# Performance work log

Measured on AMD Instinct MI355X. Metric: run time of the kernel, lower is better.

Reference implementation:

```python
import jax, jax.numpy as jnp
import numpy as np

N_NODES = 50000
N_EDGES = 800000
IN_CH = 128
HID = 128   # 2 * out_channels
OUT = 64
LN_EPS = 1e-5
L2_EPS = 1e-12


def setup_inputs() -> dict:
    key = jax.random.key(0)
    ks = jax.random.split(key, 12)
    x = jax.random.normal(ks[0], (N_NODES, IN_CH), dtype=jnp.float32)
    edge_index = jax.random.randint(ks[1], (2, N_EDGES), 0, N_NODES, dtype=jnp.int64)
    # GCNConv weights (glorot-ish scale) + bias; LayerNorm gamma/beta
    W1 = jax.random.normal(ks[2], (IN_CH, HID), dtype=jnp.float32) * (1.0 / np.sqrt(IN_CH))
    b1 = jnp.zeros((HID,), dtype=jnp.float32)
    g1 = jnp.ones((HID,), dtype=jnp.float32)
    beta1 = jnp.zeros((HID,), dtype=jnp.float32)
    W2 = jax.random.normal(ks[3], (HID, OUT), dtype=jnp.float32) * (1.0 / np.sqrt(HID))
    b2 = jnp.zeros((OUT,), dtype=jnp.float32)
    g2 = jnp.ones((OUT,), dtype=jnp.float32)
    beta2 = jnp.zeros((OUT,), dtype=jnp.float32)
    return {"x": x, "edge_index": edge_index, "W1": W1, "b1": b1, "g1": g1,
            "beta1": beta1, "W2": W2, "b2": b2, "g2": g2, "beta2": beta2}


def _layer_norm(h, gamma, beta):
    mu = jnp.mean(h, axis=-1, keepdims=True)
    var = jnp.mean(jnp.square(h - mu), axis=-1, keepdims=True)
    return (h - mu) * jax.lax.rsqrt(var + LN_EPS) * gamma + beta


def reference(x, edge_index, W1, b1, g1, beta1, W2, b2, g2, beta2):
    # Add self-loops once; compute symmetric GCN normalization (shared by both layers).
    loops = jnp.arange(N_NODES, dtype=edge_index.dtype)
    src = jnp.concatenate([edge_index[0], loops])  # [E+N]
    dst = jnp.concatenate([edge_index[1], loops])  # [E+N]
    deg = jax.ops.segment_sum(jnp.ones_like(dst, dtype=x.dtype), dst,
                              num_segments=N_NODES)
    dinv = jnp.where(deg > 0, jax.lax.rsqrt(deg), 0.0)
    norm = dinv[src] * dinv[dst]  # [E+N]

    def gcn_conv(h, W, b):
        h = h @ W                                   # [N, d_out]
        msg = h[src] * norm[:, None]                # gather + scale  [E+N, d_out]
        agg = jax.ops.segment_sum(msg, dst, num_segments=N_NODES)
        return agg + b

    h = jax.nn.relu(_layer_norm(gcn_conv(x, W1, b1), g1, beta1))
    # Dropout(0.4) is identity in eval mode (correctness baseline).
    h = jax.nn.relu(_layer_norm(gcn_conv(h, W2, b2), g2, beta2))
    nrm = jnp.sqrt(jnp.sum(jnp.square(h), axis=1, keepdims=True))
    return h / jnp.maximum(nrm, L2_EPS)
```

## Files before the change

### kernel.cpp

```cpp
#include <hip/hip_runtime.h>
#include <hip/hip_fp16.h>


#define K_DIM 128

__global__ __launch_bounds__(256) void hist_kernel(const int* __restrict__ dst,
                                                   int* counts, int E) {
    int i = blockIdx.x * 256 + threadIdx.x;
    if (i < E) atomicAdd(&counts[dst[i]], 1);
}

__global__ __launch_bounds__(256) void dinv_kernel(const int* __restrict__ counts,
                                                   float* dinv, int n) {
    int i = blockIdx.x * 256 + threadIdx.x;
    if (i < n) dinv[i] = rsqrtf((float)(counts[i] + 1));
}

__global__ __launch_bounds__(256) void scan_block_kernel(const int* __restrict__ counts,
                                                         int* row_ptr, int* partials, int N) {
    __shared__ int sm[256];
    int t = threadIdx.x;
    int i = blockIdx.x * 256 + t;
    int v = (i < N) ? counts[i] : 0;
    sm[t] = v;
    __syncthreads();
    for (int off = 1; off < 256; off <<= 1) {
        int add = (t >= off) ? sm[t - off] : 0;
        __syncthreads();
        sm[t] += add;
        __syncthreads();
    }
    if (i < N) row_ptr[i] = sm[t] - v;
    if (t == 255) partials[blockIdx.x] = sm[255];
}

__global__ __launch_bounds__(256) void scan_partials_kernel(int* partials, int NB) {
    __shared__ int sm[256];
    int t = threadIdx.x;
    int v = (t < NB) ? partials[t] : 0;
    sm[t] = v;
    __syncthreads();
    for (int off = 1; off < 256; off <<= 1) {
        int add = (t >= off) ? sm[t - off] : 0;
        __syncthreads();
        sm[t] += add;
        __syncthreads();
    }
    if (t < NB) partials[t] = sm[t] - v;
}

__global__ __launch_bounds__(256) void scan_add_kernel(int* row_ptr, const int* __restrict__ partials,
                                                       int N) {
    int i = blockIdx.x * 256 + threadIdx.x;
    if (i < N) row_ptr[i] += partials[blockIdx.x];
}

__global__ __launch_bounds__(256) void fill_kernel(const int* __restrict__ src,
                                                   const int* __restrict__ dst,
                                                   const float* __restrict__ dinv,
                                                   int* row_ptr, int* sorted_src,
                                                   float* edge_w, int E) {
    int i = blockIdx.x * 256 + threadIdx.x;
    if (i < E) {
        int d = dst[i];
        int s = src[i];
        int pos = atomicAdd(&row_ptr[d], 1);
        sorted_src[pos] = s;
        edge_w[pos] = dinv[s] * dinv[d];
    }
}

__global__ __launch_bounds__(256) void gemm1_kernel(const float* __restrict__ X,
                                                    const float* __restrict__ W,
                                                    __half* __restrict__ H, int N) {
    constexpr int COLS = 128;
    constexpr int CG = COLS / 4;
    constexpr int RG = 256 / CG;
    constexpr int RT = RG * 4;
    __shared__ float xs[RT][K_DIM + 4];

    int row0 = blockIdx.x * RT;
    for (int idx = threadIdx.x; idx < RT * K_DIM; idx += 256) {
        int r = idx >> 7;
        int c = idx & (K_DIM - 1);
        int row = row0 + r;
        xs[r][c] = (row < N) ? X[(size_t)row * K_DIM + c] : 0.0f;
    }
    __syncthreads();

    int cg = threadIdx.x % CG;
    int rg = threadIdx.x / CG;
    int col = cg * 4;

    float acc[4][4] = {};
    for (int k = 0; k < K_DIM; k += 4) {
        float4 xv0 = *(const float4*)&xs[rg * 4 + 0][k];
        float4 xv1 = *(const float4*)&xs[rg * 4 + 1][k];
        float4 xv2 = *(const float4*)&xs[rg * 4 + 2][k];
        float4 xv3 = *(const float4*)&xs[rg * 4 + 3][k];
#pragma unroll
        for (int kk = 0; kk < 4; ++kk) {
            float4 w = *(const float4*)(W + (size_t)(k + kk) * COLS + col);
            float x0 = (kk == 0) ? xv0.x : (kk == 1) ? xv0.y : (kk == 2) ? xv0.z : xv0.w;
            float x1 = (kk == 0) ? xv1.x : (kk == 1) ? xv1.y : (kk == 2) ? xv1.z : xv1.w;
            float x2 = (kk == 0) ? xv2.x : (kk == 1) ? xv2.y : (kk == 2) ? xv2.z : xv2.w;
            float x3 = (kk == 0) ? xv3.x : (kk == 1) ? xv3.y : (kk == 2) ? xv3.z : xv3.w;
            acc[0][0] = fmaf(x0, w.x, acc[0][0]); acc[0][1] = fmaf(x0, w.y, acc[0][1]);
            acc[0][2] = fmaf(x0, w.z, acc[0][2]); acc[0][3] = fmaf(x0, w.w, acc[0][3]);
            acc[1][0] = fmaf(x1, w.x, acc[1][0]); acc[1][1] = fmaf(x1, w.y, acc[1][1]);
            acc[1][2] = fmaf(x1, w.z, acc[1][2]); acc[1][3] = fmaf(x1, w.w, acc[1][3]);
            acc[2][0] = fmaf(x2, w.x, acc[2][0]); acc[2][1] = fmaf(x2, w.y, acc[2][1]);
            acc[2][2] = fmaf(x2, w.z, acc[2][2]); acc[2][3] = fmaf(x2, w.w, acc[2][3]);
            acc[3][0] = fmaf(x3, w.x, acc[3][0]); acc[3][1] = fmaf(x3, w.y, acc[3][1]);
            acc[3][2] = fmaf(x3, w.z, acc[3][2]); acc[3][3] = fmaf(x3, w.w, acc[3][3]);
        }
    }

#pragma unroll
    for (int r = 0; r < 4; ++r) {
        int row = row0 + rg * 4 + r;
        if (row < N) {
            __half2* o2 = (__half2*)(H + (size_t)row * COLS + col);
            o2[0] = __float22half2_rn(make_float2(acc[r][0], acc[r][1]));
            o2[1] = __float22half2_rn(make_float2(acc[r][2], acc[r][3]));
        }
    }
}

__global__ __launch_bounds__(256) void gather1_fused_kernel(
    const __half* __restrict__ h1, const float* __restrict__ dinv,
    const int* __restrict__ row_ptr, const int* __restrict__ counts,
    const int* __restrict__ sorted_src, const float* __restrict__ edge_w,
    const float* __restrict__ b1, const float* __restrict__ g1,
    const float* __restrict__ beta1, const float* __restrict__ W2,
    __half* __restrict__ h3, int N) {
    __shared__ float lds[4][K_DIM];
    int wave = threadIdx.x >> 6;
    int lane = threadIdx.x & 63;
    int node = blockIdx.x * 4 + wave;
    if (node >= N) return;

    float dd = dinv[node];
    float2 acc = __half22float2(((const __half2*)(h1 + (size_t)node * 128))[lane]);
    acc.x *= dd * dd; acc.y *= dd * dd;

    int end = row_ptr[node];
    int beg = end - counts[node];
    int e = beg;
    for (; e + 4 <= end; e += 4) {
        int s0 = sorted_src[e],     s1 = sorted_src[e + 1];
        int s2 = sorted_src[e + 2], s3 = sorted_src[e + 3];
        float w0 = edge_w[e],     w1 = edge_w[e + 1];
        float w2 = edge_w[e + 2], w3 = edge_w[e + 3];
        __half2 v0 = ((const __half2*)(h1 + (size_t)s0 * 128))[lane];
        __half2 v1 = ((const __half2*)(h1 + (size_t)s1 * 128))[lane];
        __half2 v2 = ((const __half2*)(h1 + (size_t)s2 * 128))[lane];
        __half2 v3 = ((const __half2*)(h1 + (size_t)s3 * 128))[lane];
        float2 f0 = __half22float2(v0), f1 = __half22float2(v1);
        float2 f2 = __half22float2(v2), f3 = __half22float2(v3);
        acc.x = fmaf(f0.x, w0, acc.x); acc.y = fmaf(f0.y, w0, acc.y);
        acc.x = fmaf(f1.x, w1, acc.x); acc.y = fmaf(f1.y, w1, acc.y);
        acc.x = fmaf(f2.x, w2, acc.x); acc.y = fmaf(f2.y, w2, acc.y);
        acc.x = fmaf(f3.x, w3, acc.x); acc.y = fmaf(f3.y, w3, acc.y);
    }
    for (; e < end; ++e) {
        int s = sorted_src[e];
        float w = edge_w[e];
        float2 f = __half22float2(((const __half2*)(h1 + (size_t)s * 128))[lane]);
        acc.x = fmaf(f.x, w, acc.x);
        acc.y = fmaf(f.y, w, acc.y);
    }

    float2 bb = ((const float2*)b1)[lane];
    acc.x += bb.x; acc.y += bb.y;
    float s = acc.x + acc.y;
    for (int off = 32; off; off >>= 1) s += __shfl_xor(s, off);
    float mu = s * (1.0f / 128.0f);
    float dx = acc.x - mu, dy = acc.y - mu;
    float q = dx * dx + dy * dy;
    for (int off = 32; off; off >>= 1) q += __shfl_xor(q, off);
    float rstd = rsqrtf(q * (1.0f / 128.0f) + 1e-5f);
    float2 gg = ((const float2*)g1)[lane];
    float2 be = ((const float2*)beta1)[lane];
    float ox = fmaxf(fmaf(dx * rstd, gg.x, be.x), 0.0f);
    float oy = fmaxf(fmaf(dy * rstd, gg.y, be.y), 0.0f);

    ((float2*)&lds[wave][0])[lane] = make_float2(ox, oy);
    float o = 0.0f;
#pragma unroll 8
    for (int k = 0; k < K_DIM; k += 4) {
        float4 vv = *(const float4*)&lds[wave][k];
        o = fmaf(vv.x, W2[(size_t)(k + 0) * 64 + lane], o);
        o = fmaf(vv.y, W2[(size_t)(k + 1) * 64 + lane], o);
        o = fmaf(vv.z, W2[(size_t)(k + 2) * 64 + lane], o);
        o = fmaf(vv.w, W2[(size_t)(k + 3) * 64 + lane], o);
    }
    h3[(size_t)node * 64 + lane] = __float2half(o);
}

__global__ __launch_bounds__(256) void gather2_fused_kernel(
    const __half* __restrict__ h3, const float* __restrict__ dinv,
    const int* __restrict__ row_ptr, const int* __restrict__ counts,
    const int* __restrict__ sorted_src, const float* __restrict__ edge_w,
    const float* __restrict__ b2, const float* __restrict__ g2,
    const float* __restrict__ beta2, float* __restrict__ out, int N) {
    int wave = threadIdx.x >> 6;
    int lane = threadIdx.x & 63;
    int node = blockIdx.x * 4 + wave;
    if (node >= N) return;

    float dd = dinv[node];
    float acc = __half2float(h3[(size_t)node * 64 + lane]) * dd * dd;

    int end = row_ptr[node];
    int beg = end - counts[node];
    int e = beg;
    for (; e + 4 <= end; e += 4) {
        int s0 = sorted_src[e],     s1 = sorted_src[e + 1];
        int s2 = sorted_src[e + 2], s3 = sorted_src[e + 3];
        float w0 = edge_w[e],     w1 = edge_w[e + 1];
        float w2 = edge_w[e + 2], w3 = edge_w[e + 3];
        float f0 = __half2float(h3[(size_t)s0 * 64 + lane]);
        float f1 = __half2float(h3[(size_t)s1 * 64 + lane]);
        float f2 = __half2float(h3[(size_t)s2 * 64 + lane]);
        float f3 = __half2float(h3[(size_t)s3 * 64 + lane]);
        acc = fmaf(f0, w0, acc);
        acc = fmaf(f1, w1, acc);
        acc = fmaf(f2, w2, acc);
        acc = fmaf(f3, w3, acc);
    }
    for (; e < end; ++e) {
        acc = fmaf(__half2float(h3[(size_t)sorted_src[e] * 64 + lane]), edge_w[e], acc);
    }

    float v = acc + b2[lane];
    float s = v;
    for (int off = 32; off; off >>= 1) s += __shfl_xor(s, off);
    float mu = s * (1.0f / 64.0f);
    float d = v - mu;
    float q = d * d;
    for (int off = 32; off; off >>= 1) q += __shfl_xor(q, off);
    float rstd = rsqrtf(q * (1.0f / 64.0f) + 1e-5f);
    float o = fmaxf(fmaf(d * rstd, g2[lane], beta2[lane]), 0.0f);
    float q2 = o * o;
    for (int off = 32; off; off >>= 1) q2 += __shfl_xor(q2, off);
    float nrm = sqrtf(q2);
    out[(size_t)node * 64 + lane] = o / fmaxf(nrm, 1e-12f);
}

extern "C" void kernel_launch(void* const* d_in, const int* in_sizes, int n_in,
                              void* d_out, int out_size, void* d_ws, size_t ws_size,
                              hipStream_t stream) {
    const float* x     = (const float*)d_in[0];
    const int*   ei    = (const int*)d_in[1];
    const float* W1    = (const float*)d_in[2];
    const float* b1    = (const float*)d_in[3];
    const float* g1    = (const float*)d_in[4];
    const float* beta1 = (const float*)d_in[5];
    const float* W2    = (const float*)d_in[6];
    const float* b2    = (const float*)d_in[7];
    const float* g2    = (const float*)d_in[8];
    const float* beta2 = (const float*)d_in[9];

    const int N = in_sizes[0] / 128;
    const int E = in_sizes[1] / 2;
    const int* src = ei;
    const int* dst = ei + E;
    float* out = (float*)d_out;

    char* p = (char*)d_ws;
    auto alloc = [&](size_t bytes) { char* r = p; p += (bytes + 255) & ~(size_t)255; return r; };
    int*    counts     = (int*)alloc((size_t)N * 4);
    int*    row_ptr    = (int*)alloc((size_t)N * 4);
    int*    partials   = (int*)alloc(256 * 4);
    float*  dinv       = (float*)alloc((size_t)N * 4);
    int*    sorted_src = (int*)alloc((size_t)E * 4);
    float*  edge_w     = (float*)alloc((size_t)E * 4);
    __half* h1         = (__half*)alloc((size_t)N * 128 * 2);
    __half* h3         = (__half*)alloc((size_t)N * 64 * 2);

    const int nb_nodes = (N + 255) / 256;
    const int nb_edges = (E + 255) / 256;
    const int nb_wave_nodes = (N + 3) / 4;

    hipMemsetAsync(counts, 0, (size_t)N * 4, stream);
    hist_kernel<<<nb_edges, 256, 0, stream>>>(dst, counts, E);
    dinv_kernel<<<nb_nodes, 256, 0, stream>>>(counts, dinv, N);
    scan_block_kernel<<<nb_nodes, 256, 0, stream>>>(counts, row_ptr, partials, N);
    scan_partials_kernel<<<1, 256, 0, stream>>>(partials, nb_nodes);
    scan_add_kernel<<<nb_nodes, 256, 0, stream>>>(row_ptr, partials, N);
    fill_kernel<<<nb_edges, 256, 0, stream>>>(src, dst, dinv, row_ptr, sorted_src, edge_w, E);

    gemm1_kernel<<<(N + 31) / 32, 256, 0, stream>>>(x, W1, h1, N);

    gather1_fused_kernel<<<nb_wave_nodes, 256, 0, stream>>>(
        h1, dinv, row_ptr, counts, sorted_src, edge_w, b1, g1, beta1, W2, h3, N);

    gather2_fused_kernel<<<nb_wave_nodes, 256, 0, stream>>>(
        h3, dinv, row_ptr, counts, sorted_src, edge_w, b2, g2, beta2, out, N);
}
```

Before: 254.8 us.

## Use MFMA GEMM, pack edges as int2, fold scan kernels, unroll gathers

Replaces the FP32 FMA GEMM for layer 1 with an fp16 MFMA 16x16x32 kernel. X is converted to half in LDS and W1 is pre-transposed to half by a small prep kernel. The dinv and scan_add kernels are merged into the scan and fill kernels, with block partials added at use time. Edge source and weight are packed into one int2 array so each edge takes one load, and the gather loops are unrolled to 8 for more memory-level parallelism. The fp16 inputs to the GEMM lower its precision.

```diff
diff --git a/kernel.cpp b/kernel.cpp
--- a/kernel.cpp
+++ b/kernel.cpp
@@ -3,6 +3,10 @@
 
 
 #define K_DIM 128
+
+typedef _Float16 f16x8 __attribute__((ext_vector_type(8)));
+typedef _Float16 f16x4 __attribute__((ext_vector_type(4)));
+typedef float f32x4 __attribute__((ext_vector_type(4)));
 
 __global__ __launch_bounds__(256) void hist_kernel(const int* __restrict__ dst,
                                                    int* counts, int E) {
@@ -10,18 +14,14 @@
     if (i < E) atomicAdd(&counts[dst[i]], 1);
 }
 
-__global__ __launch_bounds__(256) void dinv_kernel(const int* __restrict__ counts,
-                                                   float* dinv, int n) {
-    int i = blockIdx.x * 256 + threadIdx.x;
-    if (i < n) dinv[i] = rsqrtf((float)(counts[i] + 1));
-}
-
 __global__ __launch_bounds__(256) void scan_block_kernel(const int* __restrict__ counts,
-                                                         int* row_ptr, int* partials, int N) {
+                                                         int* row_ptr, int* partials,
+                                                         float* dinv, int N) {
     __shared__ int sm[256];
     int t = threadIdx.x;
     int i = blockIdx.x * 256 + t;
     int v = (i < N) ? counts[i] : 0;
+    if (i < N) dinv[i] = rsqrtf((float)(v + 1));
     sm[t] = v;
     __syncthreads();
     for (int off = 1; off < 256; off <<= 1) {
@@ -49,80 +49,80 @@
     if (t < NB) partials[t] = sm[t] - v;
 }
 
-__global__ __launch_bounds__(256) void scan_add_kernel(int* row_ptr, const int* __restrict__ partials,
-                                                       int N) {
-    int i = blockIdx.x * 256 + threadIdx.x;
-    if (i < N) row_ptr[i] += partials[blockIdx.x];
-}
-
 __global__ __launch_bounds__(256) void fill_kernel(const int* __restrict__ src,
                                                    const int* __restrict__ dst,
                                                    const float* __restrict__ dinv,
-                                                   int* row_ptr, int* sorted_src,
-                                                   float* edge_w, int E) {
+                                                   int* row_ptr,
+                                                   const int* __restrict__ partials,
+                                                   int2* edges, int E) {
     int i = blockIdx.x * 256 + threadIdx.x;
     if (i < E) {
         int d = dst[i];
         int s = src[i];
-        int pos = atomicAdd(&row_ptr[d], 1);
-        sorted_src[pos] = s;
-        edge_w[pos] = dinv[s] * dinv[d];
-    }
-}
-
-__global__ __launch_bounds__(256) void gemm1_kernel(const float* __restrict__ X,
-                                                    const float* __restrict__ W,
-                                                    __half* __restrict__ H, int N) {
-    constexpr int COLS = 128;
-    constexpr int CG = COLS / 4;
-    constexpr int RG = 256 / CG;
-    constexpr int RT = RG * 4;
-    __shared__ float xs[RT][K_DIM + 4];
-
-    int row0 = blockIdx.x * RT;
-    for (int idx = threadIdx.x; idx < RT * K_DIM; idx += 256) {
-        int r = idx >> 7;
-        int c = idx & (K_DIM - 1);
+        int pos = atomicAdd(&row_ptr[d], 1) + partials[d >> 8];
+        edges[pos] = make_int2(s, __float_as_int(dinv[s] * dinv[d]));
+    }
+}
+
+__global__ __launch_bounds__(256) void wt_prep_kernel(const float* __restrict__ W1,
+                                                      _Float16* __restrict__ WT) {
+    int idx = blockIdx.x * 256 + threadIdx.x;
+    if (idx < 128 * 128) {
+        int k = idx >> 7, j = idx & 127;
+        WT[j * 128 + k] = (_Float16)W1[idx];
+    }
+}
+
+__global__ __launch_bounds__(256) void gemm1_mfma_kernel(const float* __restrict__ X,
+                                                         const _Float16* __restrict__ WT,
+                                                         __half* __restrict__ H, int N) {
+    __shared__ _Float16 As[64][136];
+
+    int row0 = blockIdx.x * 64;
+    {
+        int r = threadIdx.x >> 2;
+        int c0 = (threadIdx.x & 3) * 32;
         int row = row0 + r;
-        xs[r][c] = (row < N) ? X[(size_t)row * K_DIM + c] : 0.0f;
+        if (row < N) {
+            const float4* srcp = (const float4*)(X + (size_t)row * 128 + c0);
+#pragma unroll
+            for (int i = 0; i < 8; ++i) {
+                float4 v = srcp[i];
+                f16x4 h = {(_Float16)v.x, (_Float16)v.y, (_Float16)v.z, (_Float16)v.w};
+                *(f16x4*)&As[r][c0 + 4 * i] = h;
+            }
+        } else {
+            f16x4 z = {};
+#pragma unroll
+            for (int i = 0; i < 8; ++i) *(f16x4*)&As[r][c0 + 4 * i] = z;
+        }
     }
     __syncthreads();
 
-    int cg = threadIdx.x % CG;
-    int rg = threadIdx.x / CG;
-    int col = cg * 4;
-
-    float acc[4][4] = {};
-    for (int k = 0; k < K_DIM; k += 4) {
-        float4 xv0 = *(const float4*)&xs[rg * 4 + 0][k];
-        float4 xv1 = *(const float4*)&xs[rg * 4 + 1][k];
-        float4 xv2 = *(const float4*)&xs[rg * 4 + 2][k];
-        float4 xv3 = *(const float4*)&xs[rg * 4 + 3][k];
-#pragma unroll
-        for (int kk = 0; kk < 4; ++kk) {
-            float4 w = *(const float4*)(W + (size_t)(k + kk) * COLS + col);
-            float x0 = (kk == 0) ? xv0.x : (kk == 1) ? xv0.y : (kk == 2) ? xv0.z : xv0.w;
-            float x1 = (kk == 0) ? xv1.x : (kk == 1) ? xv1.y : (kk == 2) ? xv1.z : xv1.w;
-            float x2 = (kk == 0) ? xv2.x : (kk == 1) ? xv2.y : (kk == 2) ? xv2.z : xv2.w;
-            float x3 = (kk == 0) ? xv3.x : (kk == 1) ? xv3.y : (kk == 2) ? xv3.z : xv3.w;
-            acc[0][0] = fmaf(x0, w.x, acc[0][0]); acc[0][1] = fmaf(x0, w.y, acc[0][1]);
-            acc[0][2] = fmaf(x0, w.z, acc[0][2]); acc[0][3] = fmaf(x0, w.w, acc[0][3]);
-            acc[1][0] = fmaf(x1, w.x, acc[1][0]); acc[1][1] = fmaf(x1, w.y, acc[1][1]);
-            acc[1][2] = fmaf(x1, w.z, acc[1][2]); acc[1][3] = fmaf(x1, w.w, acc[1][3]);
-            acc[2][0] = fmaf(x2, w.x, acc[2][0]); acc[2][1] = fmaf(x2, w.y, acc[2][1]);
-            acc[2][2] = fmaf(x2, w.z, acc[2][2]); acc[2][3] = fmaf(x2, w.w, acc[2][3]);
-            acc[3][0] = fmaf(x3, w.x, acc[3][0]); acc[3][1] = fmaf(x3, w.y, acc[3][1]);
-            acc[3][2] = fmaf(x3, w.z, acc[3][2]); acc[3][3] = fmaf(x3, w.w, acc[3][3]);
-        }
-    }
-
-#pragma unroll
-    for (int r = 0; r < 4; ++r) {
-        int row = row0 + rg * 4 + r;
-        if (row < N) {
-            __half2* o2 = (__half2*)(H + (size_t)row * COLS + col);
-            o2[0] = __float22half2_rn(make_float2(acc[r][0], acc[r][1]));
-            o2[1] = __float22half2_rn(make_float2(acc[r][2], acc[r][3]));
+    int wave = threadIdx.x >> 6;
+    int lane = threadIdx.x & 63;
+    int l15 = lane & 15;
+    int k0 = (lane >> 4) * 8;
+    int arow = wave * 16 + l15;
+
+    f32x4 acc[8] = {};
+#pragma unroll
+    for (int ks = 0; ks < 4; ++ks) {
+        f16x8 a = *(const f16x8*)&As[arow][ks * 32 + k0];
+#pragma unroll
+        for (int t = 0; t < 8; ++t) {
+            f16x8 b = *(const f16x8*)(WT + (size_t)(t * 16 + l15) * 128 + ks * 32 + k0);
+            acc[t] = __builtin_amdgcn_mfma_f32_16x16x32_f16(a, b, acc[t], 0, 0, 0);
+        }
+    }
+
+    int rbase = row0 + wave * 16 + (lane >> 4) * 4;
+#pragma unroll
+    for (int t = 0; t < 8; ++t) {
+#pragma unroll
+        for (int r = 0; r < 4; ++r) {
+            int row = rbase + r;
+            if (row < N) H[(size_t)row * 128 + t * 16 + l15] = __float2half(acc[t][r]);
         }
     }
 }
@@ -130,7 +130,7 @@
 __global__ __launch_bounds__(256) void gather1_fused_kernel(
     const __half* __restrict__ h1, const float* __restrict__ dinv,
     const int* __restrict__ row_ptr, const int* __restrict__ counts,
-    const int* __restrict__ sorted_src, const float* __restrict__ edge_w,
+    const int* __restrict__ partials, const int2* __restrict__ edges,
     const float* __restrict__ b1, const float* __restrict__ g1,
     const float* __restrict__ beta1, const float* __restrict__ W2,
     __half* __restrict__ h3, int N) {
@@ -144,29 +144,45 @@
     float2 acc = __half22float2(((const __half2*)(h1 + (size_t)node * 128))[lane]);
     acc.x *= dd * dd; acc.y *= dd * dd;
 
-    int end = row_ptr[node];
+    int end = row_ptr[node] + partials[node >> 8];
     int beg = end - counts[node];
     int e = beg;
+    for (; e + 8 <= end; e += 8) {
+        int2 rc[8];
+#pragma unroll
+        for (int i = 0; i < 8; ++i) rc[i] = edges[e + i];
+        __half2 v[8];
+#pragma unroll
+        for (int i = 0; i < 8; ++i)
+            v[i] = ((const __half2*)(h1 + (size_t)rc[i].x * 128))[lane];
+#pragma unroll
+        for (int i = 0; i < 8; ++i) {
+            float w = __int_as_float(rc[i].y);
+            float2 f = __half22float2(v[i]);
+            acc.x = fmaf(f.x, w, acc.x);
+            acc.y = fmaf(f.y, w, acc.y);
+        }
+    }
     for (; e + 4 <= end; e += 4) {
-        int s0 = sorted_src[e],     s1 = sorted_src[e + 1];
-        int s2 = sorted_src[e + 2], s3 = sorted_src[e + 3];
-        float w0 = edge_w[e],     w1 = edge_w[e + 1];
-        float w2 = edge_w[e + 2], w3 = edge_w[e + 3];
-        __half2 v0 = ((const __half2*)(h1 + (size_t)s0 * 128))[lane];
-        __half2 v1 = ((const __half2*)(h1 + (size_t)s1 * 128))[lane];
-        __half2 v2 = ((const __half2*)(h1 + (size_t)s2 * 128))[lane];
-        __half2 v3 = ((const __half2*)(h1 + (size_t)s3 * 128))[lane];
-        float2 f0 = __half22float2(v0), f1 = __half22float2(v1);
-        float2 f2 = __half22float2(v2), f3 = __half22float2(v3);
-        acc.x = fmaf(f0.x, w0, acc.x); acc.y = fmaf(f0.y, w0, acc.y);
-        acc.x = fmaf(f1.x, w1, acc.x); acc.y = fmaf(f1.y, w1, acc.y);
-        acc.x = fmaf(f2.x, w2, acc.x); acc.y = fmaf(f2.y, w2, acc.y);
-        acc.x = fmaf(f3.x, w3, acc.x); acc.y = fmaf(f3.y, w3, acc.y);
+        int2 rc[4];
+#pragma unroll
+        for (int i = 0; i < 4; ++i) rc[i] = edges[e + i];
+        __half2 v[4];
+#pragma unroll
+        for (int i = 0; i < 4; ++i)
+            v[i] = ((const __half2*)(h1 + (size_t)rc[i].x * 128))[lane];
+#pragma unroll
+        for (int i = 0; i < 4; ++i) {
+            float w = __int_as_float(rc[i].y);
+            float2 f = __half22float2(v[i]);
+            acc.x = fmaf(f.x, w, acc.x);
+            acc.y = fmaf(f.y, w, acc.y);
+        }
     }
     for (; e < end; ++e) {
-        int s = sorted_src[e];
-        float w = edge_w[e];
-        float2 f = __half22float2(((const __half2*)(h1 + (size_t)s * 128))[lane]);
+        int2 rc = edges[e];
+        float w = __int_as_float(rc.y);
+        float2 f = __half22float2(((const __half2*)(h1 + (size_t)rc.x * 128))[lane]);
         acc.x = fmaf(f.x, w, acc.x);
         acc.y = fmaf(f.y, w, acc.y);
     }
@@ -201,7 +217,7 @@
 __global__ __launch_bounds__(256) void gather2_fused_kernel(
     const __half* __restrict__ h3, const float* __restrict__ dinv,
     const int* __restrict__ row_ptr, const int* __restrict__ counts,
-    const int* __restrict__ sorted_src, const float* __restrict__ edge_w,
+    const int* __restrict__ partials, const int2* __restrict__ edges,
     const float* __restrict__ b2, const float* __restrict__ g2,
     const float* __restrict__ beta2, float* __restrict__ out, int N) {
     int wave = threadIdx.x >> 6;
@@ -212,25 +228,34 @@
     float dd = dinv[node];
     float acc = __half2float(h3[(size_t)node * 64 + lane]) * dd * dd;
 
-    int end = row_ptr[node];
+    int end = row_ptr[node] + partials[node >> 8];
     int beg = end - counts[node];
     int e = beg;
+    for (; e + 8 <= end; e += 8) {
+        int2 rc[8];
+#pragma unroll
+        for (int i = 0; i < 8; ++i) rc[i] = edges[e + i];
+        __half v[8];
+#pragma unroll
+        for (int i = 0; i < 8; ++i) v[i] = h3[(size_t)rc[i].x * 64 + lane];
+#pragma unroll
+        for (int i = 0; i < 8; ++i)
+            acc = fmaf(__half2float(v[i]), __int_as_float(rc[i].y), acc);
+    }
     for (; e + 4 <= end; e += 4) {
-        int s0 = sorted_src[e],     s1 = sorted_src[e + 1];
-        int s2 = sorted_src[e + 2], s3 = sorted_src[e + 3];
-        float w0 = edge_w[e],     w1 = edge_w[e + 1];
-        float w2 = edge_w[e + 2], w3 = edge_w[e + 3];
-        float f0 = __half2float(h3[(size_t)s0 * 64 + lane]);
-        float f1 = __half2float(h3[(size_t)s1 * 64 + lane]);
-        float f2 = __half2float(h3[(size_t)s2 * 64 + lane]);
-        float f3 = __half2float(h3[(size_t)s3 * 64 + lane]);
-        acc = fmaf(f0, w0, acc);
-        acc = fmaf(f1, w1, acc);
-        acc = fmaf(f2, w2, acc);
-        acc = fmaf(f3, w3, acc);
+        int2 rc[4];
+#pragma unroll
+        for (int i = 0; i < 4; ++i) rc[i] = edges[e + i];
+        __half v[4];
+#pragma unroll
+        for (int i = 0; i < 4; ++i) v[i] = h3[(size_t)rc[i].x * 64 + lane];
+#pragma unroll
+        for (int i = 0; i < 4; ++i)
+            acc = fmaf(__half2float(v[i]), __int_as_float(rc[i].y), acc);
     }
     for (; e < end; ++e) {
-        acc = fmaf(__half2float(h3[(size_t)sorted_src[e] * 64 + lane]), edge_w[e], acc);
+        int2 rc = edges[e];
+        acc = fmaf(__half2float(h3[(size_t)rc.x * 64 + lane]), __int_as_float(rc.y), acc);
     }
 
     float v = acc + b2[lane];
@@ -270,14 +295,14 @@
 
     char* p = (char*)d_ws;
     auto alloc = [&](size_t bytes) { char* r = p; p += (bytes + 255) & ~(size_t)255; return r; };
-    int*    counts     = (int*)alloc((size_t)N * 4);
-    int*    row_ptr    = (int*)alloc((size_t)N * 4);
-    int*    partials   = (int*)alloc(256 * 4);
-    float*  dinv       = (float*)alloc((size_t)N * 4);
-    int*    sorted_src = (int*)alloc((size_t)E * 4);
-    float*  edge_w     = (float*)alloc((size_t)E * 4);
-    __half* h1         = (__half*)alloc((size_t)N * 128 * 2);
-    __half* h3         = (__half*)alloc((size_t)N * 64 * 2);
+    int*      counts   = (int*)alloc((size_t)N * 4);
+    int*      row_ptr  = (int*)alloc((size_t)N * 4);
+    int*      partials = (int*)alloc(256 * 4);
+    float*    dinv     = (float*)alloc((size_t)N * 4);
+    int2*     edges    = (int2*)alloc((size_t)E * 8);
+    _Float16* WT       = (_Float16*)alloc(128 * 128 * 2);
+    __half*   h1       = (__half*)alloc((size_t)N * 128 * 2);
+    __half*   h3       = (__half*)alloc((size_t)N * 64 * 2);
 
     const int nb_nodes = (N + 255) / 256;
     const int nb_edges = (E + 255) / 256;
@@ -285,17 +310,16 @@
 
     hipMemsetAsync(counts, 0, (size_t)N * 4, stream);
     hist_kernel<<<nb_edges, 256, 0, stream>>>(dst, counts, E);
-    dinv_kernel<<<nb_nodes, 256, 0, stream>>>(counts, dinv, N);
-    scan_block_kernel<<<nb_nodes, 256, 0, stream>>>(counts, row_ptr, partials, N);
+    scan_block_kernel<<<nb_nodes, 256, 0, stream>>>(counts, row_ptr, partials, dinv, N);
     scan_partials_kernel<<<1, 256, 0, stream>>>(partials, nb_nodes);
-    scan_add_kernel<<<nb_nodes, 256, 0, stream>>>(row_ptr, partials, N);
-    fill_kernel<<<nb_edges, 256, 0, stream>>>(src, dst, dinv, row_ptr, sorted_src, edge_w, E);
-
-    gemm1_kernel<<<(N + 31) / 32, 256, 0, stream>>>(x, W1, h1, N);
+    fill_kernel<<<nb_edges, 256, 0, stream>>>(src, dst, dinv, row_ptr, partials, edges, E);
+
+    wt_prep_kernel<<<64, 256, 0, stream>>>(W1, WT);
+    gemm1_mfma_kernel<<<(N + 63) / 64, 256, 0, stream>>>(x, WT, h1, N);
 
     gather1_fused_kernel<<<nb_wave_nodes, 256, 0, stream>>>(
-        h1, dinv, row_ptr, counts, sorted_src, edge_w, b1, g1, beta1, W2, h3, N);
+        h1, dinv, row_ptr, counts, partials, edges, b1, g1, beta1, W2, h3, N);
 
     gather2_fused_kernel<<<nb_wave_nodes, 256, 0, stream>>>(
-        h3, dinv, row_ptr, counts, sorted_src, edge_w, b2, g2, beta2, out, N);
-}
+        h3, dinv, row_ptr, counts, partials, edges, b2, g2, beta2, out, N);
+}
```

Measured after the change: 224.9 us. 11.7% less time.
